# Kernel optimization log

Hardware: AMD Instinct MI355X
Metric: run time of the kernel (lower is better)

The kernel has to match this reference:

```python
import jax, jax.numpy as jnp
import numpy as np

N = 100000
E = 1600000
IN_C = 128
HID = 32
HEADS = 4
OUT_C = 16
NEG_SLOPE = 0.2  # PyG GATConv default


def setup_inputs() -> dict:
    key = jax.random.key(0)
    ks = jax.random.split(key, 10)
    x = jax.random.normal(ks[0], (N, IN_C), dtype=jnp.float32)
    edge_index = jax.random.randint(ks[1], (2, E), 0, N, dtype=jnp.int64)
    # Layer 1 params (heads=4, concat=True)
    s1 = 1.0 / np.sqrt(IN_C)
    W1 = jax.random.normal(ks[2], (IN_C, HEADS * HID), dtype=jnp.float32) * s1
    a_src1 = jax.random.normal(ks[3], (HEADS, HID), dtype=jnp.float32) * s1
    a_dst1 = jax.random.normal(ks[4], (HEADS, HID), dtype=jnp.float32) * s1
    b1 = jnp.zeros((HEADS * HID,), dtype=jnp.float32)
    # Layer 2 params (heads=1, concat=False)
    s2 = 1.0 / np.sqrt(HEADS * HID)
    W2 = jax.random.normal(ks[5], (HEADS * HID, OUT_C), dtype=jnp.float32) * s2
    a_src2 = jax.random.normal(ks[6], (1, OUT_C), dtype=jnp.float32) * s2
    a_dst2 = jax.random.normal(ks[7], (1, OUT_C), dtype=jnp.float32) * s2
    b2 = jnp.zeros((OUT_C,), dtype=jnp.float32)
    return {"x": x, "edge_index": edge_index, "W1": W1, "a_src1": a_src1,
            "a_dst1": a_dst1, "b1": b1, "W2": W2, "a_src2": a_src2,
            "a_dst2": a_dst2, "b2": b2}


def _gat_layer(x, src, dst, W, a_src, a_dst, b, heads, out_c, concat):
    n = x.shape[0]
    h = (x @ W).reshape(n, heads, out_c)            # [N, H, C]
    al_s = jnp.sum(h * a_src, axis=-1)              # [N, H]
    al_d = jnp.sum(h * a_dst, axis=-1)              # [N, H]
    e = al_s[src] + al_d[dst]                       # [E, H]
    e = jnp.where(e > 0, e, NEG_SLOPE * e)          # LeakyReLU(0.2)
    # segment softmax over incoming edges per destination node
    m = jax.ops.segment_max(e, dst, num_segments=n)
    ex = jnp.exp(e - m[dst])
    denom = jax.ops.segment_sum(ex, dst, num_segments=n)
    alpha = ex / denom[dst]                         # [E, H]
    msg = h[src] * alpha[:, :, None]                # [E, H, C]
    out = jax.ops.segment_sum(msg, dst, num_segments=n)  # [N, H, C]
    out = out.reshape(n, heads * out_c) if concat else out.mean(axis=1)
    return out + b


def reference(x, edge_index, W1, a_src1, a_dst1, b1, W2, a_src2, a_dst2, b2):
    n = x.shape[0]
    loops = jnp.arange(n, dtype=edge_index.dtype)
    src = jnp.concatenate([edge_index[0], loops])   # PyG adds self-loops
    dst = jnp.concatenate([edge_index[1], loops])
    h = _gat_layer(x, src, dst, W1, a_src1, a_dst1, b1, HEADS, HID, True)
    h = jax.nn.relu(h)  # dropout is identity at inference
    out = _gat_layer(h, src, dst, W2, a_src2, a_dst2, b2, 1, OUT_C, False)
    return out
```

## Files before the change

### kernel.cpp

```cpp
#include <hip/hip_runtime.h>
#include <hip/hip_fp16.h>

#define N_NODES 100000
#define N_EDGES 1600000
#define E_TOT   (N_EDGES + N_NODES)
#define NEG_SLOPE 0.2f

#define BSH   9
#define BSZ   512
#define NBKT  ((N_NODES + BSZ - 1) / BSZ)
#define CAP   10240
#define EPB   4096
#define PART_B ((E_TOT + EPB - 1) / EPB)
#define GEMM1_B ((N_NODES + 63) / 64)

__device__ __forceinline__ float lrelu(float v) { return v > 0.f ? v : NEG_SLOPE * v; }

__device__ __forceinline__ float f16lo(unsigned u) {
    return __half2float(__ushort_as_half((unsigned short)(u & 0xFFFFu)));
}
__device__ __forceinline__ float f16hi(unsigned u) {
    return __half2float(__ushort_as_half((unsigned short)(u >> 16)));
}

__global__ __launch_bounds__(256) void k_part_gemm1(
        const int* __restrict__ ei, int* __restrict__ gcur, int* __restrict__ packed,
        const float* __restrict__ x, const float* __restrict__ W1,
        const float* __restrict__ a_src, const float* __restrict__ a_dst,
        unsigned short* __restrict__ h1h, float* __restrict__ als,
        float* __restrict__ ald) {
    __shared__ __align__(16) union {
        float xs[64 * 128];
        struct { int lcnt[NBKT]; int gpos[NBKT]; int lcur[NBKT]; } p;
    } sm;
    int t = threadIdx.x;
    if (blockIdx.x < PART_B) {
        for (int i = t; i < NBKT; i += 256) sm.p.lcnt[i] = 0;
        __syncthreads();
        size_t base = (size_t)blockIdx.x * EPB;
        for (int i = t; i < EPB; i += 256) {
            size_t e = base + i;
            if (e < E_TOT) {
                int d = (e < N_EDGES) ? ei[N_EDGES + e] : (int)(e - N_EDGES);
                atomicAdd(&sm.p.lcnt[d >> BSH], 1);
            }
        }
        __syncthreads();
        for (int i = t; i < NBKT; i += 256) {
            int c = sm.p.lcnt[i];
            sm.p.gpos[i] = c ? (i * CAP + atomicAdd(&gcur[i], c)) : 0;
            sm.p.lcur[i] = 0;
        }
        __syncthreads();
        for (int i = t; i < EPB; i += 256) {
            size_t e = base + i;
            if (e < E_TOT) {
                int s, d;
                if (e < N_EDGES) { s = ei[e]; d = ei[N_EDGES + e]; }
                else             { s = (int)(e - N_EDGES); d = s; }
                int b = d >> BSH;
                int c = atomicAdd(&sm.p.lcur[b], 1);
                packed[sm.p.gpos[b] + c] = ((d & (BSZ - 1)) << 17) | s;
            }
        }
        return;
    }
    int c = t & 31, rg = t >> 5;
    int nb = (blockIdx.x - PART_B) * 64;
    const float4* xv4 = (const float4*)x;
    float4* xs4 = (float4*)sm.xs;
    size_t base4 = (size_t)nb * 32;
    const size_t lim4 = (size_t)N_NODES * 32;
#pragma unroll
    for (int i = 0; i < 8; ++i) {
        size_t g = base4 + t + i * 256;
        if (g < lim4) xs4[t + i * 256] = xv4[g];
    }
    __syncthreads();
    const float4* W1v = (const float4*)W1;
    float4 acc[8];
#pragma unroll
    for (int i = 0; i < 8; ++i) acc[i] = make_float4(0.f, 0.f, 0.f, 0.f);
#pragma unroll 4
    for (int k = 0; k < 128; ++k) {
        float4 w = W1v[k * 32 + c];
#pragma unroll
        for (int i = 0; i < 8; ++i) {
            float xv = sm.xs[(rg + 8 * i) * 128 + k];
            acc[i].x = fmaf(xv, w.x, acc[i].x);
            acc[i].y = fmaf(xv, w.y, acc[i].y);
            acc[i].z = fmaf(xv, w.z, acc[i].z);
            acc[i].w = fmaf(xv, w.w, acc[i].w);
        }
    }
    float4 as4 = ((const float4*)a_src)[c];
    float4 ad4 = ((const float4*)a_dst)[c];
#pragma unroll
    for (int i = 0; i < 8; ++i) {
        int n = nb + rg + 8 * i;
        if (n < N_NODES) {
            ushort4 hb;
            hb.x = __half_as_ushort(__float2half(acc[i].x));
            hb.y = __half_as_ushort(__float2half(acc[i].y));
            hb.z = __half_as_ushort(__float2half(acc[i].z));
            hb.w = __half_as_ushort(__float2half(acc[i].w));
            ((ushort4*)h1h)[(size_t)n * 32 + c] = hb;
        }
        float vs = acc[i].x * as4.x + acc[i].y * as4.y + acc[i].z * as4.z + acc[i].w * as4.w;
        float vd = acc[i].x * ad4.x + acc[i].y * ad4.y + acc[i].z * ad4.z + acc[i].w * ad4.w;
        vs += __shfl_down(vs, 4, 8); vs += __shfl_down(vs, 2, 8); vs += __shfl_down(vs, 1, 8);
        vd += __shfl_down(vd, 4, 8); vd += __shfl_down(vd, 2, 8); vd += __shfl_down(vd, 1, 8);
        if ((c & 7) == 0 && n < N_NODES) {
            int h = c >> 3;
            als[n * 4 + h] = vs;
            ald[n * 4 + h] = vd;
        }
    }
}

__global__ __launch_bounds__(512) void k_build(const int* __restrict__ packed,
                                               const int* __restrict__ gcur,
                                               int* __restrict__ rowptr,
                                               int* __restrict__ deg,
                                               int* __restrict__ col) {
    int t = threadIdx.x;
    int b = blockIdx.x;
    int nb = b << BSH;
    int ebeg = b * CAP;
    int eend = ebeg + gcur[b];
    __shared__ int cnt[BSZ];
    __shared__ int ps[BSZ];
    cnt[t] = 0;
    __syncthreads();
    for (int i = ebeg + t; i < eend; i += 512)
        atomicAdd(&cnt[packed[i] >> 17], 1);
    __syncthreads();
    int v = cnt[t];
    ps[t] = v;
    __syncthreads();
    for (int off = 1; off < 512; off <<= 1) {
        int u = (t >= off) ? ps[t - off] : 0;
        __syncthreads();
        ps[t] += u;
        __syncthreads();
    }
    int myofs = ebeg + ps[t] - v;
    int n = nb + t;
    if (n < N_NODES) { rowptr[n] = myofs; deg[n] = v; }
    __syncthreads();
    cnt[t] = myofs;
    __syncthreads();
    for (int i = ebeg + t; i < eend; i += 512) {
        int p = packed[i];
        int pos = atomicAdd(&cnt[p >> 17], 1);
        col[pos] = p & 0x1FFFF;
    }
}

__global__ __launch_bounds__(256) void k_agg1g2(const unsigned short* __restrict__ h1h,
                                                const float* __restrict__ als,
                                                const float* __restrict__ ald,
                                                const int* __restrict__ rowptr,
                                                const int* __restrict__ deg,
                                                const int* __restrict__ col,
                                                const float* __restrict__ b1,
                                                const float* __restrict__ W2,
                                                const float* __restrict__ as2,
                                                const float* __restrict__ ad2,
                                                unsigned short* __restrict__ h2h,
                                                float* __restrict__ als2,
                                                float* __restrict__ ald2) {
    __shared__ float sex_all[4][64 * 4];
    __shared__ int   scol_all[4][64];
    int w = threadIdx.x >> 6;
    int lane = threadIdx.x & 63;
    int n = blockIdx.x * 4 + w;
    int slot = lane >> 4, cg = lane & 15;
    int hd = cg >> 2;
    float* sex = sex_all[w];
    int* scol = scol_all[w];
    float4 ald4 = ((const float4*)ald)[n];
    int beg = rowptr[n], dtot = deg[n];
    float a0 = 0.f, a1 = 0.f, a2 = 0.f, a3 = 0.f;
    float a4 = 0.f, a5 = 0.f, a6 = 0.f, a7 = 0.f, den = 0.f;
    const float4* als4p = (const float4*)als;
    for (int base = 0; base < dtot; base += 64) {
        int cnt = min(64, dtot - base);
        int myc = 0;
        if (lane < cnt) myc = col[beg + base + lane];
        __asm__ volatile("s_waitcnt lgkmcnt(0)" ::: "memory");
        if (lane < cnt) {
            scol[lane] = myc;
            float4 as4 = als4p[myc];
            float4 e4;
            e4.x = __expf(lrelu(as4.x + ald4.x));
            e4.y = __expf(lrelu(as4.y + ald4.y));
            e4.z = __expf(lrelu(as4.z + ald4.z));
            e4.w = __expf(lrelu(as4.w + ald4.w));
            ((float4*)sex)[lane] = e4;
        }
        __asm__ volatile("s_waitcnt lgkmcnt(0)" ::: "memory");
#pragma unroll 2
        for (int q4 = 0; q4 < cnt; q4 += 4) {
            int myq = q4 + slot;
            int cq = min(myq, cnt - 1);
            int s = scol[cq];
            float ex = (myq < cnt) ? sex[cq * 4 + hd] : 0.f;
            uint4 hv = *(const uint4*)((const char*)h1h + (((size_t)s << 8) + (cg << 4)));
            a0 = fmaf(ex, f16lo(hv.x), a0);
            a1 = fmaf(ex, f16hi(hv.x), a1);
            a2 = fmaf(ex, f16lo(hv.y), a2);
            a3 = fmaf(ex, f16hi(hv.y), a3);
            a4 = fmaf(ex, f16lo(hv.z), a4);
            a5 = fmaf(ex, f16hi(hv.z), a5);
            a6 = fmaf(ex, f16lo(hv.w), a6);
            a7 = fmaf(ex, f16hi(hv.w), a7);
            den += ex;
        }
    }
    a0 += __shfl_xor(a0, 16, 64); a1 += __shfl_xor(a1, 16, 64);
    a2 += __shfl_xor(a2, 16, 64); a3 += __shfl_xor(a3, 16, 64);
    a4 += __shfl_xor(a4, 16, 64); a5 += __shfl_xor(a5, 16, 64);
    a6 += __shfl_xor(a6, 16, 64); a7 += __shfl_xor(a7, 16, 64);
    den += __shfl_xor(den, 16, 64);
    a0 += __shfl_xor(a0, 32, 64); a1 += __shfl_xor(a1, 32, 64);
    a2 += __shfl_xor(a2, 32, 64); a3 += __shfl_xor(a3, 32, 64);
    a4 += __shfl_xor(a4, 32, 64); a5 += __shfl_xor(a5, 32, 64);
    a6 += __shfl_xor(a6, 32, 64); a7 += __shfl_xor(a7, 32, 64);
    den += __shfl_xor(den, 32, 64);

    float inv = 1.0f / den;
    float4 bA = ((const float4*)b1)[2 * cg];
    float4 bB = ((const float4*)b1)[2 * cg + 1];
    float o1v[8];
    o1v[0] = fmaxf(fmaf(a0, inv, bA.x), 0.f);
    o1v[1] = fmaxf(fmaf(a1, inv, bA.y), 0.f);
    o1v[2] = fmaxf(fmaf(a2, inv, bA.z), 0.f);
    o1v[3] = fmaxf(fmaf(a3, inv, bA.w), 0.f);
    o1v[4] = fmaxf(fmaf(a4, inv, bB.x), 0.f);
    o1v[5] = fmaxf(fmaf(a5, inv, bB.y), 0.f);
    o1v[6] = fmaxf(fmaf(a6, inv, bB.z), 0.f);
    o1v[7] = fmaxf(fmaf(a7, inv, bB.w), 0.f);
    const float4* W2v = (const float4*)W2;
    int rbase = 32 * cg + slot;
    float4 p4 = make_float4(0.f, 0.f, 0.f, 0.f);
#pragma unroll
    for (int j = 0; j < 8; ++j) {
        float4 wv = W2v[rbase + j * 4];
        p4.x = fmaf(o1v[j], wv.x, p4.x);
        p4.y = fmaf(o1v[j], wv.y, p4.y);
        p4.z = fmaf(o1v[j], wv.z, p4.z);
        p4.w = fmaf(o1v[j], wv.w, p4.w);
    }
#pragma unroll
    for (int off = 1; off <= 8; off <<= 1) {
        p4.x += __shfl_xor(p4.x, off, 64);
        p4.y += __shfl_xor(p4.y, off, 64);
        p4.z += __shfl_xor(p4.z, off, 64);
        p4.w += __shfl_xor(p4.w, off, 64);
    }
    if (cg == 0) {
        ushort4 hb;
        hb.x = __half_as_ushort(__float2half(p4.x));
        hb.y = __half_as_ushort(__float2half(p4.y));
        hb.z = __half_as_ushort(__float2half(p4.z));
        hb.w = __half_as_ushort(__float2half(p4.w));
        ((ushort4*)h2h)[(size_t)n * 4 + slot] = hb;
    }
    float4 asv = ((const float4*)as2)[slot];
    float4 adv = ((const float4*)ad2)[slot];
    float vs = p4.x * asv.x + p4.y * asv.y + p4.z * asv.z + p4.w * asv.w;
    float vd = p4.x * adv.x + p4.y * adv.y + p4.z * adv.z + p4.w * adv.w;
    vs += __shfl_xor(vs, 16, 64); vs += __shfl_xor(vs, 32, 64);
    vd += __shfl_xor(vd, 16, 64); vd += __shfl_xor(vd, 32, 64);
    if (lane == 0) { als2[n] = vs; ald2[n] = vd; }
}

__global__ __launch_bounds__(256) void k_agg2(const unsigned short* __restrict__ h2h,
                                              const float* __restrict__ als,
                                              const float* __restrict__ ald,
                                              const int* __restrict__ rowptr,
                                              const int* __restrict__ deg,
                                              const int* __restrict__ col,
                                              const float* __restrict__ b2,
                                              float* __restrict__ out) {
    __shared__ float sex_all[4][64];
    __shared__ int   scol_all[4][64];
    int w = threadIdx.x >> 6;
    int lane = threadIdx.x & 63;
    int n = blockIdx.x * 4 + w;
    int slot = lane >> 2, q = lane & 3;
    float* sex = sex_all[w];
    int* scol = scol_all[w];
    float ad = ald[n];
    int beg = rowptr[n], dtot = deg[n];
    float a0 = 0.f, a1 = 0.f, a2 = 0.f, a3 = 0.f, den = 0.f;
    for (int base = 0; base < dtot; base += 64) {
        int cnt = min(64, dtot - base);
        int myc = 0;
        if (lane < cnt) myc = col[beg + base + lane];
        __asm__ volatile("s_waitcnt lgkmcnt(0)" ::: "memory");
        if (lane < cnt) {
            scol[lane] = myc;
            sex[lane] = __expf(lrelu(als[myc] + ad));
        }
        __asm__ volatile("s_waitcnt lgkmcnt(0)" ::: "memory");
#pragma unroll 2
        for (int q16 = 0; q16 < cnt; q16 += 16) {
            int myq = q16 + slot;
            int cq = min(myq, cnt - 1);
            int s = scol[cq];
            float ex = (myq < cnt) ? sex[cq] : 0.f;
            uint2 hv = *(const uint2*)((const char*)h2h + ((size_t)s * 32u + (q << 3)));
            a0 = fmaf(ex, f16lo(hv.x), a0);
            a1 = fmaf(ex, f16hi(hv.x), a1);
            a2 = fmaf(ex, f16lo(hv.y), a2);
            a3 = fmaf(ex, f16hi(hv.y), a3);
            den += ex;
        }
    }
#pragma unroll
    for (int off = 4; off <= 32; off <<= 1) {
        a0 += __shfl_xor(a0, off, 64);
        a1 += __shfl_xor(a1, off, 64);
        a2 += __shfl_xor(a2, off, 64);
        a3 += __shfl_xor(a3, off, 64);
        den += __shfl_xor(den, off, 64);
    }
    if (slot == 0) {
        float inv = 1.0f / den;
        float4 b4 = ((const float4*)b2)[q];
        float4 o;
        o.x = fmaf(a0, inv, b4.x);
        o.y = fmaf(a1, inv, b4.y);
        o.z = fmaf(a2, inv, b4.z);
        o.w = fmaf(a3, inv, b4.w);
        ((float4*)out)[(size_t)n * 4 + q] = o;
    }
}

extern "C" void kernel_launch(void* const* d_in, const int* in_sizes, int n_in,
                              void* d_out, int out_size, void* d_ws, size_t ws_size,
                              hipStream_t stream) {
    const float* x   = (const float*)d_in[0];
    const int*   ei  = (const int*)d_in[1];
    const float* W1  = (const float*)d_in[2];
    const float* as1 = (const float*)d_in[3];
    const float* ad1 = (const float*)d_in[4];
    const float* b1  = (const float*)d_in[5];
    const float* W2  = (const float*)d_in[6];
    const float* as2 = (const float*)d_in[7];
    const float* ad2 = (const float*)d_in[8];
    const float* b2  = (const float*)d_in[9];
    float* out = (float*)d_out;

    char* ws = (char*)d_ws;
    size_t off = 0;
    auto alloc = [&](size_t bytes) -> void* {
        void* p = ws + off;
        off += (bytes + 255) & ~(size_t)255;
        return p;
    };
    unsigned short* h1h = (unsigned short*)alloc((size_t)N_NODES * 128 * 2);
    float* als1v = (float*)alloc((size_t)N_NODES * 4 * 4);
    float* ald1v = (float*)alloc((size_t)N_NODES * 4 * 4);
    unsigned short* h2h = (unsigned short*)alloc((size_t)N_NODES * 16 * 2);
    float* als2v = (float*)alloc((size_t)N_NODES * 4);
    float* ald2v = (float*)alloc((size_t)N_NODES * 4);
    int* rowptr  = (int*)alloc((size_t)N_NODES * 4);
    int* degv    = (int*)alloc((size_t)N_NODES * 4);
    int* gcur    = (int*)alloc((size_t)NBKT * 4);
    int* packed  = (int*)alloc((size_t)NBKT * CAP * 4);
    int* colA    = (int*)alloc((size_t)NBKT * CAP * 4);

    hipMemsetAsync(gcur, 0, (size_t)NBKT * 4, stream);
    k_part_gemm1<<<PART_B + GEMM1_B, 256, 0, stream>>>(ei, gcur, packed,
                                                       x, W1, as1, ad1, h1h, als1v, ald1v);
    k_build<<<NBKT, 512, 0, stream>>>(packed, gcur, rowptr, degv, colA);
    k_agg1g2<<<N_NODES / 4, 256, 0, stream>>>(h1h, als1v, ald1v, rowptr, degv, colA,
                                              b1, W2, as2, ad2, h2h, als2v, ald2v);
    k_agg2<<<N_NODES / 4, 256, 0, stream>>>(h2h, als2v, ald2v, rowptr, degv, colA, b2, out);
}
```

Baseline: 343.0 us.

## Map one node per 16-lane group in both aggregation kernels

Both aggregation kernels now give each 16-lane group its own destination node, where before a whole 64-lane wavefront handled one node. This processes four nodes per wave and drops the shared-memory staging of column indices and exp weights. In layer 1 each lane walks the edges serially, prefetching the next column index and computing its own head's exp inline. The layer-2 projection uses a transpose-style shuffle reduction within 16 lanes. The intent is to cut wasted lanes and barriers for low-degree nodes (about 17 edges per node on average). The trade-off is less memory-level parallelism per node and a serial dependency chain per edge in layer 1.

```diff
diff --git a/kernel.cpp b/kernel.cpp
--- a/kernel.cpp
+++ b/kernel.cpp
@@ -170,65 +170,32 @@
                                                 unsigned short* __restrict__ h2h,
                                                 float* __restrict__ als2,
                                                 float* __restrict__ ald2) {
-    __shared__ float sex_all[4][64 * 4];
-    __shared__ int   scol_all[4][64];
     int w = threadIdx.x >> 6;
     int lane = threadIdx.x & 63;
-    int n = blockIdx.x * 4 + w;
-    int slot = lane >> 4, cg = lane & 15;
+    int g = lane >> 4, cg = lane & 15;
     int hd = cg >> 2;
-    float* sex = sex_all[w];
-    int* scol = scol_all[w];
-    float4 ald4 = ((const float4*)ald)[n];
+    int n = blockIdx.x * 16 + w * 4 + g;
+    float adh = ald[n * 4 + hd];
     int beg = rowptr[n], dtot = deg[n];
     float a0 = 0.f, a1 = 0.f, a2 = 0.f, a3 = 0.f;
     float a4 = 0.f, a5 = 0.f, a6 = 0.f, a7 = 0.f, den = 0.f;
-    const float4* als4p = (const float4*)als;
-    for (int base = 0; base < dtot; base += 64) {
-        int cnt = min(64, dtot - base);
-        int myc = 0;
-        if (lane < cnt) myc = col[beg + base + lane];
-        __asm__ volatile("s_waitcnt lgkmcnt(0)" ::: "memory");
-        if (lane < cnt) {
-            scol[lane] = myc;
-            float4 as4 = als4p[myc];
-            float4 e4;
-            e4.x = __expf(lrelu(as4.x + ald4.x));
-            e4.y = __expf(lrelu(as4.y + ald4.y));
-            e4.z = __expf(lrelu(as4.z + ald4.z));
-            e4.w = __expf(lrelu(as4.w + ald4.w));
-            ((float4*)sex)[lane] = e4;
-        }
-        __asm__ volatile("s_waitcnt lgkmcnt(0)" ::: "memory");
-#pragma unroll 2
-        for (int q4 = 0; q4 < cnt; q4 += 4) {
-            int myq = q4 + slot;
-            int cq = min(myq, cnt - 1);
-            int s = scol[cq];
-            float ex = (myq < cnt) ? sex[cq * 4 + hd] : 0.f;
-            uint4 hv = *(const uint4*)((const char*)h1h + (((size_t)s << 8) + (cg << 4)));
-            a0 = fmaf(ex, f16lo(hv.x), a0);
-            a1 = fmaf(ex, f16hi(hv.x), a1);
-            a2 = fmaf(ex, f16lo(hv.y), a2);
-            a3 = fmaf(ex, f16hi(hv.y), a3);
-            a4 = fmaf(ex, f16lo(hv.z), a4);
-            a5 = fmaf(ex, f16hi(hv.z), a5);
-            a6 = fmaf(ex, f16lo(hv.w), a6);
-            a7 = fmaf(ex, f16hi(hv.w), a7);
-            den += ex;
-        }
-    }
-    a0 += __shfl_xor(a0, 16, 64); a1 += __shfl_xor(a1, 16, 64);
-    a2 += __shfl_xor(a2, 16, 64); a3 += __shfl_xor(a3, 16, 64);
-    a4 += __shfl_xor(a4, 16, 64); a5 += __shfl_xor(a5, 16, 64);
-    a6 += __shfl_xor(a6, 16, 64); a7 += __shfl_xor(a7, 16, 64);
-    den += __shfl_xor(den, 16, 64);
-    a0 += __shfl_xor(a0, 32, 64); a1 += __shfl_xor(a1, 32, 64);
-    a2 += __shfl_xor(a2, 32, 64); a3 += __shfl_xor(a3, 32, 64);
-    a4 += __shfl_xor(a4, 32, 64); a5 += __shfl_xor(a5, 32, 64);
-    a6 += __shfl_xor(a6, 32, 64); a7 += __shfl_xor(a7, 32, 64);
-    den += __shfl_xor(den, 32, 64);
-
+    int sv = col[beg];
+    for (int e = 0; e < dtot; ++e) {
+        int s = sv;
+        sv = col[beg + min(e + 1, dtot - 1)];
+        float al = als[s * 4 + hd];
+        uint4 hv = *(const uint4*)((const char*)h1h + (((size_t)s << 8) + (cg << 4)));
+        float ex = __expf(lrelu(al + adh));
+        a0 = fmaf(ex, f16lo(hv.x), a0);
+        a1 = fmaf(ex, f16hi(hv.x), a1);
+        a2 = fmaf(ex, f16lo(hv.y), a2);
+        a3 = fmaf(ex, f16hi(hv.y), a3);
+        a4 = fmaf(ex, f16lo(hv.z), a4);
+        a5 = fmaf(ex, f16hi(hv.z), a5);
+        a6 = fmaf(ex, f16lo(hv.w), a6);
+        a7 = fmaf(ex, f16hi(hv.w), a7);
+        den += ex;
+    }
     float inv = 1.0f / den;
     float4 bA = ((const float4*)b1)[2 * cg];
     float4 bB = ((const float4*)b1)[2 * cg + 1];
@@ -242,38 +209,76 @@
     o1v[6] = fmaxf(fmaf(a6, inv, bB.z), 0.f);
     o1v[7] = fmaxf(fmaf(a7, inv, bB.w), 0.f);
     const float4* W2v = (const float4*)W2;
-    int rbase = 32 * cg + slot;
-    float4 p4 = make_float4(0.f, 0.f, 0.f, 0.f);
+    float4 p0 = make_float4(0.f, 0.f, 0.f, 0.f);
+    float4 p1 = make_float4(0.f, 0.f, 0.f, 0.f);
+    float4 p2 = make_float4(0.f, 0.f, 0.f, 0.f);
+    float4 p3 = make_float4(0.f, 0.f, 0.f, 0.f);
 #pragma unroll
     for (int j = 0; j < 8; ++j) {
-        float4 wv = W2v[rbase + j * 4];
-        p4.x = fmaf(o1v[j], wv.x, p4.x);
-        p4.y = fmaf(o1v[j], wv.y, p4.y);
-        p4.z = fmaf(o1v[j], wv.z, p4.z);
-        p4.w = fmaf(o1v[j], wv.w, p4.w);
-    }
-#pragma unroll
-    for (int off = 1; off <= 8; off <<= 1) {
-        p4.x += __shfl_xor(p4.x, off, 64);
-        p4.y += __shfl_xor(p4.y, off, 64);
-        p4.z += __shfl_xor(p4.z, off, 64);
-        p4.w += __shfl_xor(p4.w, off, 64);
-    }
-    if (cg == 0) {
+        float ov = o1v[j];
+        int rb = (8 * cg + j) * 4;
+        float4 w0 = W2v[rb + 0];
+        float4 w1 = W2v[rb + 1];
+        float4 w2 = W2v[rb + 2];
+        float4 w3 = W2v[rb + 3];
+        p0.x = fmaf(ov, w0.x, p0.x); p0.y = fmaf(ov, w0.y, p0.y);
+        p0.z = fmaf(ov, w0.z, p0.z); p0.w = fmaf(ov, w0.w, p0.w);
+        p1.x = fmaf(ov, w1.x, p1.x); p1.y = fmaf(ov, w1.y, p1.y);
+        p1.z = fmaf(ov, w1.z, p1.z); p1.w = fmaf(ov, w1.w, p1.w);
+        p2.x = fmaf(ov, w2.x, p2.x); p2.y = fmaf(ov, w2.y, p2.y);
+        p2.z = fmaf(ov, w2.z, p2.z); p2.w = fmaf(ov, w2.w, p2.w);
+        p3.x = fmaf(ov, w3.x, p3.x); p3.y = fmaf(ov, w3.y, p3.y);
+        p3.z = fmaf(ov, w3.z, p3.z); p3.w = fmaf(ov, w3.w, p3.w);
+    }
+    bool b8 = (cg & 8) != 0;
+    float4 s0, s1;
+    {
+        float4 q0 = b8 ? p2 : p0, q1 = b8 ? p3 : p1;
+        float4 r0, r1, r2, r3;
+        r0.x = __shfl_xor(p0.x, 8, 16); r0.y = __shfl_xor(p0.y, 8, 16);
+        r0.z = __shfl_xor(p0.z, 8, 16); r0.w = __shfl_xor(p0.w, 8, 16);
+        r1.x = __shfl_xor(p1.x, 8, 16); r1.y = __shfl_xor(p1.y, 8, 16);
+        r1.z = __shfl_xor(p1.z, 8, 16); r1.w = __shfl_xor(p1.w, 8, 16);
+        r2.x = __shfl_xor(p2.x, 8, 16); r2.y = __shfl_xor(p2.y, 8, 16);
+        r2.z = __shfl_xor(p2.z, 8, 16); r2.w = __shfl_xor(p2.w, 8, 16);
+        r3.x = __shfl_xor(p3.x, 8, 16); r3.y = __shfl_xor(p3.y, 8, 16);
+        r3.z = __shfl_xor(p3.z, 8, 16); r3.w = __shfl_xor(p3.w, 8, 16);
+        float4 u0 = b8 ? r2 : r0, u1 = b8 ? r3 : r1;
+        s0.x = q0.x + u0.x; s0.y = q0.y + u0.y; s0.z = q0.z + u0.z; s0.w = q0.w + u0.w;
+        s1.x = q1.x + u1.x; s1.y = q1.y + u1.y; s1.z = q1.z + u1.z; s1.w = q1.w + u1.w;
+    }
+    bool b4 = (cg & 4) != 0;
+    float4 h2v;
+    {
+        float4 q = b4 ? s1 : s0;
+        float4 r0, r1;
+        r0.x = __shfl_xor(s0.x, 4, 16); r0.y = __shfl_xor(s0.y, 4, 16);
+        r0.z = __shfl_xor(s0.z, 4, 16); r0.w = __shfl_xor(s0.w, 4, 16);
+        r1.x = __shfl_xor(s1.x, 4, 16); r1.y = __shfl_xor(s1.y, 4, 16);
+        r1.z = __shfl_xor(s1.z, 4, 16); r1.w = __shfl_xor(s1.w, 4, 16);
+        float4 u = b4 ? r1 : r0;
+        h2v.x = q.x + u.x; h2v.y = q.y + u.y; h2v.z = q.z + u.z; h2v.w = q.w + u.w;
+    }
+    h2v.x += __shfl_xor(h2v.x, 2, 16); h2v.y += __shfl_xor(h2v.y, 2, 16);
+    h2v.z += __shfl_xor(h2v.z, 2, 16); h2v.w += __shfl_xor(h2v.w, 2, 16);
+    h2v.x += __shfl_xor(h2v.x, 1, 16); h2v.y += __shfl_xor(h2v.y, 1, 16);
+    h2v.z += __shfl_xor(h2v.z, 1, 16); h2v.w += __shfl_xor(h2v.w, 1, 16);
+    int Q = cg >> 2;
+    if ((cg & 3) == 0) {
         ushort4 hb;
-        hb.x = __half_as_ushort(__float2half(p4.x));
-        hb.y = __half_as_ushort(__float2half(p4.y));
-        hb.z = __half_as_ushort(__float2half(p4.z));
-        hb.w = __half_as_ushort(__float2half(p4.w));
-        ((ushort4*)h2h)[(size_t)n * 4 + slot] = hb;
-    }
-    float4 asv = ((const float4*)as2)[slot];
-    float4 adv = ((const float4*)ad2)[slot];
-    float vs = p4.x * asv.x + p4.y * asv.y + p4.z * asv.z + p4.w * asv.w;
-    float vd = p4.x * adv.x + p4.y * adv.y + p4.z * adv.z + p4.w * adv.w;
-    vs += __shfl_xor(vs, 16, 64); vs += __shfl_xor(vs, 32, 64);
-    vd += __shfl_xor(vd, 16, 64); vd += __shfl_xor(vd, 32, 64);
-    if (lane == 0) { als2[n] = vs; ald2[n] = vd; }
+        hb.x = __half_as_ushort(__float2half(h2v.x));
+        hb.y = __half_as_ushort(__float2half(h2v.y));
+        hb.z = __half_as_ushort(__float2half(h2v.z));
+        hb.w = __half_as_ushort(__float2half(h2v.w));
+        ((ushort4*)h2h)[(size_t)n * 4 + Q] = hb;
+    }
+    float4 asv = ((const float4*)as2)[Q];
+    float4 adv = ((const float4*)ad2)[Q];
+    float vs = h2v.x * asv.x + h2v.y * asv.y + h2v.z * asv.z + h2v.w * asv.w;
+    float vd = h2v.x * adv.x + h2v.y * adv.y + h2v.z * adv.z + h2v.w * adv.w;
+    vs += __shfl_xor(vs, 4, 16); vs += __shfl_xor(vs, 8, 16);
+    vd += __shfl_xor(vd, 4, 16); vd += __shfl_xor(vd, 8, 16);
+    if (cg == 0) { als2[n] = vs; ald2[n] = vd; }
 }
 
 __global__ __launch_bounds__(256) void k_agg2(const unsigned short* __restrict__ h2h,
@@ -284,50 +289,33 @@
                                               const int* __restrict__ col,
                                               const float* __restrict__ b2,
                                               float* __restrict__ out) {
-    __shared__ float sex_all[4][64];
-    __shared__ int   scol_all[4][64];
     int w = threadIdx.x >> 6;
     int lane = threadIdx.x & 63;
-    int n = blockIdx.x * 4 + w;
-    int slot = lane >> 2, q = lane & 3;
-    float* sex = sex_all[w];
-    int* scol = scol_all[w];
-    float ad = ald[n];
+    int g = lane >> 4, cg = lane & 15;
+    int es = cg >> 2, q = cg & 3;
+    int n = blockIdx.x * 16 + w * 4 + g;
+    float adn = ald[n];
     int beg = rowptr[n], dtot = deg[n];
     float a0 = 0.f, a1 = 0.f, a2 = 0.f, a3 = 0.f, den = 0.f;
-    for (int base = 0; base < dtot; base += 64) {
-        int cnt = min(64, dtot - base);
-        int myc = 0;
-        if (lane < cnt) myc = col[beg + base + lane];
-        __asm__ volatile("s_waitcnt lgkmcnt(0)" ::: "memory");
-        if (lane < cnt) {
-            scol[lane] = myc;
-            sex[lane] = __expf(lrelu(als[myc] + ad));
-        }
-        __asm__ volatile("s_waitcnt lgkmcnt(0)" ::: "memory");
-#pragma unroll 2
-        for (int q16 = 0; q16 < cnt; q16 += 16) {
-            int myq = q16 + slot;
-            int cq = min(myq, cnt - 1);
-            int s = scol[cq];
-            float ex = (myq < cnt) ? sex[cq] : 0.f;
-            uint2 hv = *(const uint2*)((const char*)h2h + ((size_t)s * 32u + (q << 3)));
-            a0 = fmaf(ex, f16lo(hv.x), a0);
-            a1 = fmaf(ex, f16hi(hv.x), a1);
-            a2 = fmaf(ex, f16lo(hv.y), a2);
-            a3 = fmaf(ex, f16hi(hv.y), a3);
-            den += ex;
-        }
-    }
-#pragma unroll
-    for (int off = 4; off <= 32; off <<= 1) {
-        a0 += __shfl_xor(a0, off, 64);
-        a1 += __shfl_xor(a1, off, 64);
-        a2 += __shfl_xor(a2, off, 64);
-        a3 += __shfl_xor(a3, off, 64);
-        den += __shfl_xor(den, off, 64);
-    }
-    if (slot == 0) {
+    for (int base = 0; base < dtot; base += 4) {
+        int myq = base + es;
+        int cq = min(myq, dtot - 1);
+        int s = col[beg + cq];
+        float ex = (myq < dtot) ? __expf(lrelu(als[s] + adn)) : 0.f;
+        uint2 hv = *(const uint2*)((const char*)h2h + ((size_t)s * 32u + (q << 3)));
+        a0 = fmaf(ex, f16lo(hv.x), a0);
+        a1 = fmaf(ex, f16hi(hv.x), a1);
+        a2 = fmaf(ex, f16lo(hv.y), a2);
+        a3 = fmaf(ex, f16hi(hv.y), a3);
+        den += ex;
+    }
+    a0 += __shfl_xor(a0, 4, 16); a1 += __shfl_xor(a1, 4, 16);
+    a2 += __shfl_xor(a2, 4, 16); a3 += __shfl_xor(a3, 4, 16);
+    den += __shfl_xor(den, 4, 16);
+    a0 += __shfl_xor(a0, 8, 16); a1 += __shfl_xor(a1, 8, 16);
+    a2 += __shfl_xor(a2, 8, 16); a3 += __shfl_xor(a3, 8, 16);
+    den += __shfl_xor(den, 8, 16);
+    if (es == 0) {
         float inv = 1.0f / den;
         float4 b4 = ((const float4*)b2)[q];
         float4 o;
@@ -377,7 +365,7 @@
     k_part_gemm1<<<PART_B + GEMM1_B, 256, 0, stream>>>(ei, gcur, packed,
                                                        x, W1, as1, ad1, h1h, als1v, ald1v);
     k_build<<<NBKT, 512, 0, stream>>>(packed, gcur, rowptr, degv, colA);
-    k_agg1g2<<<N_NODES / 4, 256, 0, stream>>>(h1h, als1v, ald1v, rowptr, degv, colA,
-                                              b1, W2, as2, ad2, h2h, als2v, ald2v);
-    k_agg2<<<N_NODES / 4, 256, 0, stream>>>(h2h, als2v, ald2v, rowptr, degv, colA, b2, out);
-}
+    k_agg1g2<<<N_NODES / 16, 256, 0, stream>>>(h1h, als1v, ald1v, rowptr, degv, colA,
+                                               b1, W2, as2, ad2, h2h, als2v, ald2v);
+    k_agg2<<<N_NODES / 16, 256, 0, stream>>>(h2h, als2v, ald2v, rowptr, degv, colA, b2, out);
+}
```

After: 348.4 us. About the same (+1.6%).
